# Performance work log

Measured on AMD Instinct MI355X. Metric: run time of the kernel, lower is better.

The kernel has to match this reference:

```python
import jax, jax.numpy as jnp
import numpy as np

L = 12; D = 768; H = 12; HD = D // H
P = 16; IMG = 224; NPATCH = (IMG // P) ** 2
NCLS = 1000; B = 32
GAMMA = 0.01; MIN_TOKENS = 16; EPS = 1e-6
SCALE = HD ** -0.5


def _ln(x, w, b, eps=1e-6):
    mu = x.mean(-1, keepdims=True)
    var = ((x - mu) ** 2).mean(-1, keepdims=True)
    return (x - mu) * jax.lax.rsqrt(var + eps) * w + b


def setup_inputs() -> dict:
    key = jax.random.key(0)
    ks = jax.random.split(key, 16)
    s = 0.02
    rn = lambda k, shape: jax.random.normal(k, shape, jnp.float32) * s
    return {
        'x': jax.random.normal(ks[0], (B, 3, IMG, IMG), jnp.float32),
        'patch_w': rn(ks[1], (D, 3, P, P)),
        'patch_b': jnp.zeros((D,), jnp.float32),
        'cls_token': rn(ks[2], (1, 1, D)),
        'pos_embed': rn(ks[3], (1, NPATCH + 1, D)),
        'ln1_w': jnp.ones((L, D), jnp.float32), 'ln1_b': jnp.zeros((L, D), jnp.float32),
        'qkv_w': rn(ks[4], (L, D, 3 * D)), 'qkv_b': jnp.zeros((L, 3 * D), jnp.float32),
        'proj_w': rn(ks[5], (L, D, D)), 'proj_b': jnp.zeros((L, D), jnp.float32),
        'ln2_w': jnp.ones((L, D), jnp.float32), 'ln2_b': jnp.zeros((L, D), jnp.float32),
        'fc1_w': rn(ks[6], (L, D, 4 * D)), 'fc1_b': jnp.zeros((L, 4 * D), jnp.float32),
        'fc2_w': rn(ks[7], (L, 4 * D, D)), 'fc2_b': jnp.zeros((L, D), jnp.float32),
        'norm_w': jnp.ones((D,), jnp.float32), 'norm_b': jnp.zeros((D,), jnp.float32),
        'head_w': rn(ks[8], (D, NCLS)), 'head_b': jnp.zeros((NCLS,), jnp.float32),
    }


def _block(x, i, ln1_w, ln1_b, qkv_w, qkv_b, proj_w, proj_b, ln2_w, ln2_b, fc1_w, fc1_b, fc2_w, fc2_b):
    Bb, Ntok, _ = x.shape
    xn = _ln(x, ln1_w[i], ln1_b[i])
    qkv = (xn @ qkv_w[i] + qkv_b[i]).reshape(Bb, Ntok, 3, H, HD)
    qkv = qkv.transpose(2, 0, 3, 1, 4)  # [3, B, H, N, hd]
    q, k, v = qkv[0], qkv[1], qkv[2]
    # full N x N attention matrix, materialized as in the original module
    attn = jax.nn.softmax(jnp.einsum('bhqd,bhkd->bhqk', q, k) * SCALE, axis=-1)
    out = jnp.einsum('bhqk,bhkd->bhqd', attn, v)
    out = out.transpose(0, 2, 1, 3).reshape(Bb, Ntok, D) @ proj_w[i] + proj_b[i]
    x = x + out
    h = _ln(x, ln2_w[i], ln2_b[i])
    h = jax.nn.gelu(h @ fc1_w[i] + fc1_b[i], approximate=False)
    x = x + (h @ fc2_w[i] + fc2_b[i])
    return x, attn, v


def _importance(attn, v, eps):
    # Jacobian proxy: d(CLS)/d(patch_j) ~ attn[CLS->j] * ||v_j||
    v_norm = jnp.linalg.norm(v, axis=-1)            # [B, H, N]
    jac = attn[:, :, 0, 1:] * v_norm[:, :, 1:]       # [B, H, Npatch]
    importance = jac.mean(axis=(0, 1))               # batch-shared [Npatch]
    mass = importance.sum()
    rho = importance.std() / (importance.mean() + eps)
    return importance, mass, rho


def _keep_ratio(rho, mass, prev_mass, gamma, eps):
    drift = jnp.abs(mass - prev_mass) / (prev_mass + eps)
    return jnp.clip(1.0 - gamma * rho * (1.0 + drift), 0.0, 1.0)


def _select(importance, n_keep):
    _, idx = jax.lax.top_k(importance, n_keep)
    idx = jnp.sort(idx) + 1  # shift past CLS
    return jnp.concatenate([jnp.zeros((1,), idx.dtype), idx])  # always keep CLS


def reference(x, patch_w, patch_b, cls_token, pos_embed, ln1_w, ln1_b, qkv_w, qkv_b,
              proj_w, proj_b, ln2_w, ln2_b, fc1_w, fc1_b, fc2_w, fc2_b,
              norm_w, norm_b, head_w, head_b):
    Bb = x.shape[0]
    feat = jax.lax.conv_general_dilated(x, patch_w, (P, P), 'VALID',
                                        dimension_numbers=('NCHW', 'OIHW', 'NCHW'))
    feat = feat.reshape(Bb, D, NPATCH).transpose(0, 2, 1) + patch_b  # [B, 196, D]
    xx = jnp.concatenate([jnp.broadcast_to(cls_token, (Bb, 1, D)), feat], axis=1) + pos_embed
    N = NPATCH
    prev_mass = None
    for i in range(L):
        xx, attn, v = _block(xx, i, ln1_w, ln1_b, qkv_w, qkv_b, proj_w, proj_b,
                             ln2_w, ln2_b, fc1_w, fc1_b, fc2_w, fc2_b)
        if N <= MIN_TOKENS:
            prev_mass = None
            continue
        imp, mass, rho = _importance(attn, v, EPS)
        if prev_mass is not None:
            kr = float(_keep_ratio(rho, mass, prev_mass, GAMMA, EPS))
            n_next = max(MIN_TOKENS, int(N * kr))
        else:
            n_next = N
        if n_next < N:
            keep_idx = _select(imp, n_next)
            xx = jnp.take(xx, keep_idx, axis=1)
            N = n_next
        prev_mass = mass
    xx = _ln(xx, norm_w, norm_b)
    return xx[:, 0] @ head_w + head_b
```

## Files before the change

### kernel.cpp

```cpp
#include <hip/hip_runtime.h>
#include <math.h>

#define DEV_INLINE __device__ __forceinline__

constexpr int BB     = 32;
constexpr int DMODEL = 768;
constexpr int NHEAD  = 12;
constexpr int NPATCH = 196;
constexpr int NTOK   = 197;
constexpr int NLAYER = 12;
constexpr int NCLASS = 1000;
constexpr int MTOT   = BB * NTOK;

typedef __attribute__((ext_vector_type(4))) float f32x4;
typedef __attribute__((ext_vector_type(8))) short bf16x8;

DEV_INLINE void split2(float x, unsigned short& hi, unsigned short& lo) {
    unsigned u = __builtin_bit_cast(unsigned, x);
    unsigned r = (u + 0x7FFFu + ((u >> 16) & 1u)) >> 16;
    hi = (unsigned short)r;
    float fh = __builtin_bit_cast(float, r << 16);
    float l = x - fh;
    unsigned ul = __builtin_bit_cast(unsigned, l);
    lo = (unsigned short)((ul + 0x7FFFu + ((ul >> 16) & 1u)) >> 16);
}

DEV_INLINE unsigned split_pack(float x) {
    unsigned short h, l; split2(x, h, l);
    return (unsigned)h | ((unsigned)l << 16);
}

DEV_INLINE void gload16(const unsigned short* g, unsigned short* l) {
    __builtin_amdgcn_global_load_lds(
        (const __attribute__((address_space(1))) unsigned int*)g,
        (__attribute__((address_space(3))) unsigned int*)l, 16, 0, 0);
}

DEV_INLINE float block_reduce_sum(float v, float* sbuf) {
    #pragma unroll
    for (int off = 32; off > 0; off >>= 1) v += __shfl_down(v, off, 64);
    int lane = threadIdx.x & 63, w = threadIdx.x >> 6;
    __syncthreads();
    if (lane == 0) sbuf[w] = v;
    __syncthreads();
    return sbuf[0] + sbuf[1] + sbuf[2] + sbuf[3];
}

__global__ void state_init(int* nTokPtr, int* prevValidPtr) {
    *nTokPtr = NTOK;
    *prevValidPtr = 0;
}

__global__ __launch_bounds__(256)
void cls_init(const float* __restrict__ cls, const float* __restrict__ pos,
              float* __restrict__ tok) {
    int b = blockIdx.x;
    for (int i = threadIdx.x; i < DMODEL; i += 256)
        tok[(size_t)b * NTOK * DMODEL + i] = cls[i] + pos[i];
}

__global__ __launch_bounds__(256)
void wconv_patch(const float* __restrict__ src, unsigned short* __restrict__ hi,
                 unsigned short* __restrict__ lo) {
    int id = blockIdx.x * 256 + threadIdx.x;
    if (id >= 768 * 96) return;
    int n = id / 96, ch = id % 96;
    int k = ch * 8;
    float4 a = *(const float4*)(src + (size_t)n * 768 + k);
    float4 b = *(const float4*)(src + (size_t)n * 768 + k + 4);
    unsigned short h[8], l[8];
    split2(a.x,h[0],l[0]); split2(a.y,h[1],l[1]); split2(a.z,h[2],l[2]); split2(a.w,h[3],l[3]);
    split2(b.x,h[4],l[4]); split2(b.y,h[5],l[5]); split2(b.z,h[6],l[6]); split2(b.w,h[7],l[7]);
    int npanel = n >> 7, c = n & 127;
    int kbi = k >> 5, chunk = (k >> 3) & 3;
    size_t base = ((size_t)npanel * 24 + kbi) * 4096
                + c * 32 + ((chunk ^ ((c >> 1) & 3)) << 3);
    bf16x8 hv, lv;
    #pragma unroll
    for (int j = 0; j < 8; ++j) { hv[j] = (short)h[j]; lv[j] = (short)l[j]; }
    *(bf16x8*)(hi + base) = hv;
    *(bf16x8*)(lo + base) = lv;
}

constexpr size_t WOFF_QKV  = 0;
constexpr size_t WOFF_PROJ = (size_t)768 * 2304;
constexpr size_t WOFF_FC1  = WOFF_PROJ + (size_t)768 * 768;
constexpr size_t WOFF_FC2  = WOFF_FC1 + (size_t)768 * 3072;
constexpr size_t WTOTAL    = WOFF_FC2 + (size_t)3072 * 768;

__global__ __launch_bounds__(256)
void wconv_layer(const float* __restrict__ qkvw, const float* __restrict__ projw,
                 const float* __restrict__ fc1w, const float* __restrict__ fc2w,
                 unsigned short* __restrict__ hi, unsigned short* __restrict__ lo) {
    __shared__ float tile[32][33];
    int bid = blockIdx.x;
    const float* src; int Kd, Nd; size_t dofs;
    if (bid < 1728)      { src = qkvw;  Kd = 768;  Nd = 2304; dofs = WOFF_QKV; }
    else if (bid < 2304) { bid -= 1728; src = projw; Kd = 768;  Nd = 768;  dofs = WOFF_PROJ; }
    else if (bid < 4608) { bid -= 2304; src = fc1w;  Kd = 768;  Nd = 3072; dofs = WOFF_FC1; }
    else                 { bid -= 4608; src = fc2w;  Kd = 3072; Nd = 768;  dofs = WOFF_FC2; }
    const int nkb = Kd >> 5;
    int ntx = Nd / 32;
    int n0 = (bid % ntx) * 32, k0 = (bid / ntx) * 32;
    int tx = threadIdx.x & 31, ty = threadIdx.x >> 5;
    #pragma unroll
    for (int i = 0; i < 32; i += 8)
        tile[ty + i][tx] = src[(size_t)(k0 + ty + i) * Nd + n0 + tx];
    __syncthreads();
    int t = threadIdx.x;
    if (t < 128) {
        int nl = t >> 2, chunk = t & 3;
        unsigned short h[8], l[8];
        #pragma unroll
        for (int j = 0; j < 8; ++j) split2(tile[chunk * 8 + j][nl], h[j], l[j]);
        int n = n0 + nl, k = k0 + chunk * 8;
        int npanel = n >> 7, c = n & 127;
        int kbi = k >> 5;
        size_t base = dofs + ((size_t)npanel * nkb + kbi) * 4096
                    + c * 32 + ((chunk ^ ((c >> 1) & 3)) << 3);
        bf16x8 hv, lv;
        #pragma unroll
        for (int j = 0; j < 8; ++j) { hv[j] = (short)h[j]; lv[j] = (short)l[j]; }
        *(bf16x8*)(hi + base) = hv;
        *(bf16x8*)(lo + base) = lv;
    }
}

template<int ASRC, int EPI>
__global__ __launch_bounds__(256)
void mfma_gemm(const void* __restrict__ A, int lda,
               const unsigned short* __restrict__ Wht,
               const unsigned short* __restrict__ Wlt,
               const float* __restrict__ bias,
               const float* __restrict__ resid,
               void* __restrict__ C, int ldc,
               int K, int Mtot, int gm, int gn,
               const int* __restrict__ nTokPtr) {
    const int nTok = (ASRC == 0) ? *nTokPtr : NTOK;
    int nb = gm * gn;
    int o = blockIdx.x;
    int q8 = nb >> 3, r8 = nb & 7;
    int xcd = o & 7, wi = o >> 3;
    int fin = (xcd < r8 ? xcd * (q8 + 1) : r8 * (q8 + 1) + (xcd - r8) * q8) + wi;
    int bm = fin / gn, bn = fin - bm * gn;
    const int m0 = bm * 128, n0 = bn * 128;
    if (m0 >= Mtot) return;
    if (ASRC == 0) {
        int ts = m0 % NTOK;
        if (!(ts < nTok || ts + 128 > NTOK)) return;
    }
    __shared__ unsigned short Ah[4096], Al[4096], Bh[4096], Bl[4096];
    const int tid = threadIdx.x;
    const int lane = tid & 63, wid = tid >> 6;
    const int wm = wid >> 1, wn = wid & 1;
    const int fr = lane & 15, fg = lane >> 4;

    f32x4 acc[4][4];
    #pragma unroll
    for (int i = 0; i < 4; ++i)
        #pragma unroll
        for (int j = 0; j < 4; ++j) acc[i][j] = (f32x4){0.f, 0.f, 0.f, 0.f};

    const int arow = tid >> 1;
    const int acp  = (tid & 1) * 2;
    const int am = m0 + arow;
    bool aval = am < Mtot;
    if (ASRC == 0) aval = aval && (am % NTOK) < nTok;
    size_t abase;
    if (ASRC == 0) abase = (size_t)am * lda;
    else {
        int b = am / NPATCH, pp = am - b * NPATCH;
        int py = pp / 14, px = pp - py * 14;
        abase = (size_t)b * (3 * 224 * 224) + (size_t)(py * 16) * 224 + px * 16;
    }
    const int axor = (arow >> 1) & 3;
    const int aoff0 = arow * 32 + ((acp ^ axor) << 3);
    const int aoff1 = arow * 32 + (((acp + 1) ^ axor) << 3);
    const int nkb = K >> 5;
    const int wbase = wid * 512;
    const int g8 = tid * 8;

    for (int kbi = 0; kbi < nkb; ++kbi) {
        const int kb = kbi << 5;
        {
            size_t tb = ((size_t)bn * nkb + kbi) * 4096;
            gload16(Wht + tb + g8,        &Bh[wbase]);
            gload16(Wht + tb + g8 + 2048, &Bh[wbase + 2048]);
            gload16(Wlt + tb + g8,        &Bl[wbase]);
            gload16(Wlt + tb + g8 + 2048, &Bl[wbase + 2048]);
        }
        unsigned ph[8], pl[8];
        if (ASRC == 0) {
            unsigned u[16] = {0,0,0,0,0,0,0,0,0,0,0,0,0,0,0,0};
            if (aval) {
                const unsigned* ap = (const unsigned*)A + abase + kb + acp * 8;
                *(uint4*)&u[0]  = *(const uint4*)ap;
                *(uint4*)&u[4]  = *(const uint4*)(ap + 4);
                *(uint4*)&u[8]  = *(const uint4*)(ap + 8);
                *(uint4*)&u[12] = *(const uint4*)(ap + 12);
            }
            #pragma unroll
            for (int j = 0; j < 8; ++j) {
                unsigned a = u[2 * j], b = u[2 * j + 1];
                ph[j] = (a & 0xffffu) | (b << 16);
                pl[j] = (a >> 16) | (b & 0xffff0000u);
            }
        } else {
            float f[16] = {0,0,0,0,0,0,0,0,0,0,0,0,0,0,0,0};
            if (aval) {
                int k = kb + acp * 8;
                size_t off = abase + (size_t)(k >> 8) * (224 * 224)
                           + (size_t)((k >> 4) & 15) * 224;
                *(float4*)&f[0]  = *(const float4*)((const float*)A + off);
                *(float4*)&f[4]  = *(const float4*)((const float*)A + off + 4);
                *(float4*)&f[8]  = *(const float4*)((const float*)A + off + 8);
                *(float4*)&f[12] = *(const float4*)((const float*)A + off + 12);
            }
            #pragma unroll
            for (int j = 0; j < 8; ++j) {
                unsigned short h0, l0, h1, l1;
                split2(f[2 * j], h0, l0); split2(f[2 * j + 1], h1, l1);
                ph[j] = (unsigned)h0 | ((unsigned)h1 << 16);
                pl[j] = (unsigned)l0 | ((unsigned)l1 << 16);
            }
        }
        *(uint4*)&Ah[aoff0] = *(uint4*)&ph[0];
        *(uint4*)&Ah[aoff1] = *(uint4*)&ph[4];
        *(uint4*)&Al[aoff0] = *(uint4*)&pl[0];
        *(uint4*)&Al[aoff1] = *(uint4*)&pl[4];
        __syncthreads();
        bf16x8 ah[4], al4[4], bh4[4], bl4[4];
        #pragma unroll
        for (int i = 0; i < 4; ++i) {
            int row = wm * 64 + i * 16 + fr;
            int aoff = row * 32 + ((fg ^ ((row >> 1) & 3)) << 3);
            ah[i]  = *(const bf16x8*)&Ah[aoff];
            al4[i] = *(const bf16x8*)&Al[aoff];
            int col = wn * 64 + i * 16 + fr;
            int boff = col * 32 + ((fg ^ ((col >> 1) & 3)) << 3);
            bh4[i] = *(const bf16x8*)&Bh[boff];
            bl4[i] = *(const bf16x8*)&Bl[boff];
        }
        #pragma unroll
        for (int i = 0; i < 4; ++i)
            #pragma unroll
            for (int j = 0; j < 4; ++j) {
                acc[i][j] = __builtin_amdgcn_mfma_f32_16x16x32_bf16(ah[i],  bh4[j], acc[i][j], 0, 0, 0);
                acc[i][j] = __builtin_amdgcn_mfma_f32_16x16x32_bf16(ah[i],  bl4[j], acc[i][j], 0, 0, 0);
                acc[i][j] = __builtin_amdgcn_mfma_f32_16x16x32_bf16(al4[i], bh4[j], acc[i][j], 0, 0, 0);
            }
        __syncthreads();
    }
    #pragma unroll
    for (int i = 0; i < 4; ++i) {
        #pragma unroll
        for (int j = 0; j < 4; ++j) {
            #pragma unroll
            for (int e = 0; e < 4; ++e) {
                int m = m0 + wm * 64 + i * 16 + fg * 4 + e;
                int n = n0 + wn * 64 + j * 16 + fr;
                if (m >= Mtot) continue;
                if (ASRC == 0 && (m % NTOK) >= nTok) continue;
                float v = acc[i][j][e] + bias[n];
                if constexpr (EPI == 0) {
                    ((unsigned*)C)[(size_t)m * ldc + n] = split_pack(v);
                } else if constexpr (EPI == 1) {
                    ((float*)C)[(size_t)m * ldc + n] = v + resid[(size_t)m * ldc + n];
                } else if constexpr (EPI == 2) {
                    v = 0.5f * v * (1.0f + erff(v * 0.70710678118654752f));
                    ((unsigned*)C)[(size_t)m * ldc + n] = split_pack(v);
                } else {
                    int b = m / NPATCH, pp = m - b * NPATCH;
                    v += resid[(size_t)(1 + pp) * DMODEL + n];
                    ((float*)C)[((size_t)b * NTOK + 1 + pp) * DMODEL + n] = v;
                }
            }
        }
    }
}

__global__ __launch_bounds__(256)
void ln_tok(const float* __restrict__ X, unsigned* __restrict__ Y,
            const float* __restrict__ w, const float* __restrict__ b,
            const int* __restrict__ nTokPtr) {
    int m = blockIdx.x;
    if ((m % NTOK) >= *nTokPtr) return;
    __shared__ float sbuf[4];
    const float* x = X + (size_t)m * DMODEL;
    int tid = threadIdx.x;
    float v[3];
    #pragma unroll
    for (int i = 0; i < 3; i++) v[i] = x[tid + i * 256];
    float mu = block_reduce_sum(v[0] + v[1] + v[2], sbuf) * (1.0f / 768.0f);
    float d2 = 0.f;
    #pragma unroll
    for (int i = 0; i < 3; i++) { float d = v[i] - mu; d2 = fmaf(d, d, d2); }
    float var = block_reduce_sum(d2, sbuf) * (1.0f / 768.0f);
    float rstd = rsqrtf(var + 1e-6f);
    #pragma unroll
    for (int i = 0; i < 3; i++) {
        int idx = tid + i * 256;
        float y = (v[i] - mu) * rstd * w[idx] + b[idx];
        Y[(size_t)m * DMODEL + idx] = split_pack(y);
    }
}

__global__ __launch_bounds__(256)
void ln_cls(const float* __restrict__ X, float* __restrict__ Y,
            const float* __restrict__ w, const float* __restrict__ b) {
    int bb = blockIdx.x;
    __shared__ float sbuf[4];
    const float* x = X + (size_t)bb * NTOK * DMODEL;
    int tid = threadIdx.x;
    float v[3];
    #pragma unroll
    for (int i = 0; i < 3; i++) v[i] = x[tid + i * 256];
    float mu = block_reduce_sum(v[0] + v[1] + v[2], sbuf) * (1.0f / 768.0f);
    float d2 = 0.f;
    #pragma unroll
    for (int i = 0; i < 3; i++) { float d = v[i] - mu; d2 = fmaf(d, d, d2); }
    float var = block_reduce_sum(d2, sbuf) * (1.0f / 768.0f);
    float rstd = rsqrtf(var + 1e-6f);
    #pragma unroll
    for (int i = 0; i < 3; i++) {
        int idx = tid + i * 256;
        Y[(size_t)bb * DMODEL + idx] = (v[i] - mu) * rstd * w[idx] + b[idx];
    }
}

__global__ __launch_bounds__(256)
void attn_v3(const unsigned* __restrict__ qkv, unsigned* __restrict__ outu,
             float* __restrict__ jacg, const int* __restrict__ nTokPtr) {
    const int nTok = *nTokPtr;
    const int bh = blockIdx.x;
    const int b = bh / NHEAD, h = bh % NHEAD;
    const int q0 = blockIdx.y * 32;
    if (q0 >= nTok) return;
    __shared__ unsigned short Kh[64 * 64], Kl[64 * 64];
    __shared__ unsigned short Vth[64 * 64], Vtl[64 * 64];
    __shared__ unsigned short Ph[32 * 64], Pl[32 * 64];
    __shared__ float Ss[32][68];
    __shared__ float mrow[32], lrow[32], frow[32];
    __shared__ float s0row[256], vnrow[256];
    __shared__ float vnpart[64][4];
    const int tid = threadIdx.x;
    const int lane = tid & 63, wv = tid >> 6;
    const int fr = lane & 15, fg = lane >> 4;
    const int qh = wv >> 1, xh = wv & 1;
    const unsigned* base = qkv + (size_t)b * NTOK * 2304 + (size_t)h * 64;

    {
        unsigned* Qu = (unsigned*)&Ss[0][0];
        int r = tid >> 3, fc = tid & 7;
        int q = q0 + r;
        uint4 v = make_uint4(0,0,0,0), w = make_uint4(0,0,0,0);
        if (q < nTok) {
            v = *(const uint4*)(base + (size_t)q * 2304 + fc * 8);
            w = *(const uint4*)(base + (size_t)q * 2304 + fc * 8 + 4);
        }
        *(uint4*)&Qu[r * 68 + fc * 8] = v;
        *(uint4*)&Qu[r * 68 + fc * 8 + 4] = w;
    }
    if (tid < 32) { mrow[tid] = -INFINITY; lrow[tid] = 0.f; frow[tid] = 1.f; }
    __syncthreads();
    bf16x8 qah[2], qal[2];
    {
        const unsigned* Qu = (const unsigned*)&Ss[0][0];
        int r = qh * 16 + fr;
        #pragma unroll
        for (int s = 0; s < 2; ++s)
            #pragma unroll
            for (int i = 0; i < 8; ++i) {
                unsigned u = Qu[r * 68 + s * 32 + fg * 8 + i];
                qah[s][i] = (short)(u & 0xffffu);
                qal[s][i] = (short)(u >> 16);
            }
    }
    f32x4 oacc[2] = {{0,0,0,0},{0,0,0,0}};
    const int njt = (nTok + 63) >> 6;
    const int sj = tid & 63, sdh = tid >> 6;

    for (int jt = 0; jt < njt; ++jt) {
        const int jb = jt * 64;
        __syncthreads();
        {
            int j = jb + sj;
            uint4 ku[4], vu[4];
            if (j < nTok) {
                const unsigned* kr = base + (size_t)j * 2304 + 768 + sdh * 16;
                const unsigned* vr = base + (size_t)j * 2304 + 1536 + sdh * 16;
                ku[0] = *(const uint4*)kr;       ku[1] = *(const uint4*)(kr + 4);
                ku[2] = *(const uint4*)(kr + 8); ku[3] = *(const uint4*)(kr + 12);
                vu[0] = *(const uint4*)vr;       vu[1] = *(const uint4*)(vr + 4);
                vu[2] = *(const uint4*)(vr + 8); vu[3] = *(const uint4*)(vr + 12);
            } else {
                ku[0]=ku[1]=ku[2]=ku[3] = make_uint4(0,0,0,0);
                vu[0]=vu[1]=vu[2]=vu[3] = make_uint4(0,0,0,0);
            }
            const unsigned* kw = (const unsigned*)ku;
            bf16x8 kh0, kh1, kl0, kl1;
            #pragma unroll
            for (int i = 0; i < 8; ++i) {
                kh0[i] = (short)(kw[i] & 0xffffu);     kl0[i] = (short)(kw[i] >> 16);
                kh1[i] = (short)(kw[8 + i] & 0xffffu); kl1[i] = (short)(kw[8 + i] >> 16);
            }
            int c0 = sdh * 2;
            int ko0 = sj * 64 + ((c0 ^ (sj & 7)) << 3);
            int ko1 = sj * 64 + (((c0 + 1) ^ (sj & 7)) << 3);
            *(bf16x8*)&Kh[ko0] = kh0; *(bf16x8*)&Kh[ko1] = kh1;
            *(bf16x8*)&Kl[ko0] = kl0; *(bf16x8*)&Kl[ko1] = kl1;
            const unsigned* vw = (const unsigned*)vu;
            float pn = 0.f;
            #pragma unroll
            for (int i = 0; i < 16; ++i) {
                unsigned u = vw[i];
                int d = sdh * 16 + i;
                int si = d * 64 + (((sj >> 3) ^ (d & 7)) << 3) + (sj & 7);
                Vth[si] = (unsigned short)(u & 0xffffu);
                Vtl[si] = (unsigned short)(u >> 16);
                if (q0 == 0) {
                    float vf = __builtin_bit_cast(float, u << 16)
                             + __builtin_bit_cast(float, u & 0xffff0000u);
                    pn = fmaf(vf, vf, pn);
                }
            }
            if (q0 == 0) vnpart[sj][sdh] = pn;
        }
        __syncthreads();
        {
            f32x4 sacc[2] = {{0,0,0,0},{0,0,0,0}};
            #pragma unroll
            for (int s = 0; s < 2; ++s)
                #pragma unroll
                for (int t = 0; t < 2; ++t) {
                    int j = xh * 32 + t * 16 + fr;
                    int off = j * 64 + (((s * 4 + fg) ^ (j & 7)) << 3);
                    bf16x8 kbh = *(const bf16x8*)&Kh[off];
                    bf16x8 kbl = *(const bf16x8*)&Kl[off];
                    sacc[t] = __builtin_amdgcn_mfma_f32_16x16x32_bf16(qah[s], kbh, sacc[t], 0, 0, 0);
                    sacc[t] = __builtin_amdgcn_mfma_f32_16x16x32_bf16(qah[s], kbl, sacc[t], 0, 0, 0);
                    sacc[t] = __builtin_amdgcn_mfma_f32_16x16x32_bf16(qal[s], kbh, sacc[t], 0, 0, 0);
                }
            #pragma unroll
            for (int t = 0; t < 2; ++t)
                #pragma unroll
                for (int e = 0; e < 4; ++e) {
                    int q = q0 + qh * 16 + fg * 4 + e;
                    int j = jb + xh * 32 + t * 16 + fr;
                    Ss[qh * 16 + fg * 4 + e][xh * 32 + t * 16 + fr] =
                        (q < nTok && j < nTok) ? sacc[t][e] * 0.125f : -INFINITY;
                }
        }
        __syncthreads();
        {
            int q = tid >> 3, s = tid & 7;
            bool rowok = (q0 + q) < nTok;
            float4 va = *(const float4*)&Ss[q][s * 8];
            float4 vb = *(const float4*)&Ss[q][s * 8 + 4];
            if (q0 == 0 && q == 0) {
                *(float4*)&s0row[jb + s * 8] = va;
                *(float4*)&s0row[jb + s * 8 + 4] = vb;
            }
            float mx = fmaxf(fmaxf(fmaxf(va.x, va.y), fmaxf(va.z, va.w)),
                             fmaxf(fmaxf(vb.x, vb.y), fmaxf(vb.z, vb.w)));
            #pragma unroll
            for (int o = 1; o < 8; o <<= 1) mx = fmaxf(mx, __shfl_xor(mx, o));
            float mold = mrow[q];
            float mnew = fmaxf(mold, mx);
            float e[8];
            float sum = 0.f;
            if (rowok) {
                e[0] = expf(va.x - mnew); e[1] = expf(va.y - mnew);
                e[2] = expf(va.z - mnew); e[3] = expf(va.w - mnew);
                e[4] = expf(vb.x - mnew); e[5] = expf(vb.y - mnew);
                e[6] = expf(vb.z - mnew); e[7] = expf(vb.w - mnew);
                sum = ((e[0] + e[1]) + (e[2] + e[3])) + ((e[4] + e[5]) + (e[6] + e[7]));
            } else {
                #pragma unroll
                for (int i = 0; i < 8; ++i) e[i] = 0.f;
            }
            #pragma unroll
            for (int o = 1; o < 8; o <<= 1) sum += __shfl_xor(sum, o);
            bf16x8 ph, pl;
            #pragma unroll
            for (int i = 0; i < 8; ++i) {
                unsigned u = __builtin_bit_cast(unsigned, e[i]);
                ph[i] = (short)(u >> 16);
                float r = e[i] - __builtin_bit_cast(float, u & 0xffff0000u);
                pl[i] = (short)(__builtin_bit_cast(unsigned, r) >> 16);
            }
            int poff = q * 64 + ((s ^ (q & 7)) << 3);
            *(bf16x8*)&Ph[poff] = ph;
            *(bf16x8*)&Pl[poff] = pl;
            if (s == 0 && rowok) {
                float f = expf(mold - mnew);
                lrow[q] = lrow[q] * f + sum;
                mrow[q] = mnew;
                frow[q] = f;
            }
            if (q0 == 0 && tid < 64) {
                int jj = jb + tid;
                if (jj < nTok)
                    vnrow[jj] = sqrtf(vnpart[tid][0] + vnpart[tid][1]
                                    + vnpart[tid][2] + vnpart[tid][3]);
            }
        }
        __syncthreads();
        {
            float fe[4];
            #pragma unroll
            for (int e = 0; e < 4; ++e) fe[e] = frow[qh * 16 + fg * 4 + e];
            #pragma unroll
            for (int t = 0; t < 2; ++t)
                #pragma unroll
                for (int e = 0; e < 4; ++e) oacc[t][e] *= fe[e];
            #pragma unroll
            for (int s = 0; s < 2; ++s) {
                int pr = qh * 16 + fr;
                int poff = pr * 64 + (((s * 4 + fg) ^ (pr & 7)) << 3);
                bf16x8 pah = *(const bf16x8*)&Ph[poff];
                bf16x8 pal = *(const bf16x8*)&Pl[poff];
                #pragma unroll
                for (int t = 0; t < 2; ++t) {
                    int d = xh * 32 + t * 16 + fr;
                    int voff = d * 64 + (((s * 4 + fg) ^ (d & 7)) << 3);
                    bf16x8 vbh = *(const bf16x8*)&Vth[voff];
                    bf16x8 vbl = *(const bf16x8*)&Vtl[voff];
                    oacc[t] = __builtin_amdgcn_mfma_f32_16x16x32_bf16(pah, vbh, oacc[t], 0, 0, 0);
                    oacc[t] = __builtin_amdgcn_mfma_f32_16x16x32_bf16(pah, vbl, oacc[t], 0, 0, 0);
                    oacc[t] = __builtin_amdgcn_mfma_f32_16x16x32_bf16(pal, vbh, oacc[t], 0, 0, 0);
                }
            }
        }
    }
    #pragma unroll
    for (int e = 0; e < 4; ++e) {
        int qr = qh * 16 + fg * 4 + e;
        int q = q0 + qr;
        if (q < nTok) {
            float inv = 1.0f / lrow[qr];
            #pragma unroll
            for (int t = 0; t < 2; ++t) {
                int n = h * 64 + xh * 32 + t * 16 + fr;
                outu[((size_t)b * NTOK + q) * DMODEL + n] = split_pack(oacc[t][e] * inv);
            }
        }
    }
    if (q0 == 0) {
        float m0f = mrow[0], l0 = lrow[0];
        for (int j = 1 + tid; j < nTok; j += 256)
            jacg[(size_t)bh * NPATCH + (j - 1)] = (expf(s0row[j] - m0f) / l0) * vnrow[j];
    }
}

__global__ __launch_bounds__(256)
void decide_kernel(const float* __restrict__ jac,
                   int* __restrict__ nTokPtr, int* __restrict__ nTokNextPtr,
                   int* __restrict__ keepIdx, float* __restrict__ prevMassPtr,
                   int* __restrict__ prevValidPtr) {
    const int nTok = *nTokPtr;
    const int N = nTok - 1;
    const int tid = threadIdx.x;
    if (N <= 16) {
        if (tid == 0) { *prevValidPtr = 0; *nTokNextPtr = nTok; }
        for (int t = tid; t < nTok; t += 256) keepIdx[t] = t;
        return;
    }
    __shared__ float impF[NPATCH];
    __shared__ int   sel[NPATCH];
    __shared__ int   s_next;
    for (int j = tid; j < N; j += 256) {
        double s = 0.0;
        for (int r = 0; r < BB * NHEAD; r++) s += (double)jac[(size_t)r * NPATCH + j];
        impF[j] = (float)(s * (1.0 / 384.0));
    }
    __syncthreads();
    if (tid == 0) {
        double ms = 0.0;
        for (int j = 0; j < N; j++) ms += (double)impF[j];
        float massF = (float)ms;
        float meanF = (float)(ms / (double)N);
        double vs = 0.0;
        for (int j = 0; j < N; j++) { double d = (double)impF[j] - (double)meanF; vs += d * d; }
        float stdF = (float)sqrt(vs / (double)N);
        float rho = stdF / (meanF + 1e-6f);
        int nnext;
        if (*prevValidPtr != 0) {
            float pm = *prevMassPtr;
            float drift = fabsf(massF - pm) / (pm + 1e-6f);
            float kr = 1.0f - 0.01f * rho * (1.0f + drift);
            kr = fminf(fmaxf(kr, 0.0f), 1.0f);
            int t = (int)((double)N * (double)kr);
            nnext = t < 16 ? 16 : t;
        } else {
            nnext = N;
        }
        *prevMassPtr = massF;
        *prevValidPtr = 1;
        s_next = nnext;
        *nTokNextPtr = nnext + 1;
    }
    __syncthreads();
    int nnext = s_next;
    if (nnext < N) {
        for (int j = tid; j < N; j += 256) {
            float vj = impF[j];
            int rank = 0;
            for (int i = 0; i < N; i++) {
                float vi = impF[i];
                rank += (vi > vj || (vi == vj && i < j)) ? 1 : 0;
            }
            sel[j] = (rank < nnext) ? 1 : 0;
        }
        __syncthreads();
        if (tid == 0) {
            int c = 1;
            keepIdx[0] = 0;
            for (int j = 0; j < N; j++) if (sel[j]) keepIdx[c++] = j + 1;
        }
    } else {
        for (int t = tid; t < nTok; t += 256) keepIdx[t] = t;
    }
}

__global__ __launch_bounds__(192)
void gather_kernel(const float* __restrict__ src, float* __restrict__ dst,
                   const int* __restrict__ keepIdx,
                   const int* __restrict__ nTokNextPtr, int* __restrict__ nTokPtr) {
    int nn = *nTokNextPtr;
    int m = blockIdx.x;
    int b = m / NTOK, t = m - b * NTOK;
    if (t < nn) {
        int s = keepIdx[t];
        const float4* sp = (const float4*)(src + ((size_t)b * NTOK + s) * DMODEL);
        float4* dp = (float4*)(dst + ((size_t)b * NTOK + t) * DMODEL);
        dp[threadIdx.x] = sp[threadIdx.x];
    }
    if (m == 0 && threadIdx.x == 0) *nTokPtr = nn;
}

__global__ __launch_bounds__(256)
void head_kernel(const float* __restrict__ lnC, const float* __restrict__ W,
                 const float* __restrict__ hb, float* __restrict__ out) {
    int b = blockIdx.x;
    int n = blockIdx.y * 256 + threadIdx.x;
    __shared__ float xs[DMODEL];
    for (int i = threadIdx.x; i < DMODEL; i += 256) xs[i] = lnC[(size_t)b * DMODEL + i];
    __syncthreads();
    if (n < NCLASS) {
        float acc = hb[n];
        for (int d = 0; d < DMODEL; d++) acc = fmaf(xs[d], W[(size_t)d * NCLASS + n], acc);
        out[(size_t)b * NCLASS + n] = acc;
    }
}

extern "C" void kernel_launch(void* const* d_in, const int* in_sizes, int n_in,
                              void* d_out, int out_size, void* d_ws, size_t ws_size,
                              hipStream_t stream) {
    const float* x       = (const float*)d_in[0];
    const float* patch_w = (const float*)d_in[1];
    const float* patch_b = (const float*)d_in[2];
    const float* cls_tok = (const float*)d_in[3];
    const float* pos     = (const float*)d_in[4];
    const float* ln1_w   = (const float*)d_in[5];
    const float* ln1_b   = (const float*)d_in[6];
    const float* qkv_w   = (const float*)d_in[7];
    const float* qkv_b   = (const float*)d_in[8];
    const float* proj_w  = (const float*)d_in[9];
    const float* proj_b  = (const float*)d_in[10];
    const float* ln2_w   = (const float*)d_in[11];
    const float* ln2_b   = (const float*)d_in[12];
    const float* fc1_w   = (const float*)d_in[13];
    const float* fc1_b   = (const float*)d_in[14];
    const float* fc2_w   = (const float*)d_in[15];
    const float* fc2_b   = (const float*)d_in[16];
    const float* norm_w  = (const float*)d_in[17];
    const float* norm_b  = (const float*)d_in[18];
    const float* head_w  = (const float*)d_in[19];
    const float* head_b  = (const float*)d_in[20];
    float* out = (float*)d_out;

    char* ws = (char*)d_ws;
    size_t off = 0;
    auto alloc = [&](size_t nbytes) {
        char* p = ws + off;
        off += ((nbytes + 255) / 256) * 256;
        return p;
    };
    float* tokA = (float*)alloc((size_t)MTOT * DMODEL * 4);
    float* tokB = (float*)alloc((size_t)MTOT * DMODEL * 4);
    char* uni = alloc((size_t)MTOT * 3072 * 4);
    unsigned* qkvb = (unsigned*)uni;
    unsigned* hbu = (unsigned*)uni;
    unsigned* xnu  = (unsigned*)alloc((size_t)MTOT * DMODEL * 4);
    unsigned* outu = (unsigned*)alloc((size_t)MTOT * DMODEL * 4);
    unsigned short* whi = (unsigned short*)alloc(WTOTAL * 2);
    unsigned short* wlo = (unsigned short*)alloc(WTOTAL * 2);
    unsigned short* wphi = (unsigned short*)alloc((size_t)768 * 768 * 2);
    unsigned short* wplo = (unsigned short*)alloc((size_t)768 * 768 * 2);
    float* jac  = (float*)alloc((size_t)BB * NHEAD * NPATCH * 4);
    float* lnC  = (float*)alloc((size_t)BB * DMODEL * 4);
    float* prevMass = (float*)alloc(32);
    int* ints = (int*)alloc(1024);
    int* nTokP = ints; int* nTokNextP = ints + 1; int* prevValidP = ints + 2;
    int* keepIdx = ints + 4;

    dim3 blk(256);
    state_init<<<dim3(1), dim3(1), 0, stream>>>(nTokP, prevValidP);
    wconv_patch<<<dim3(288), blk, 0, stream>>>(patch_w, wphi, wplo);
    cls_init<<<dim3(BB), blk, 0, stream>>>(cls_tok, pos, tokA);
    mfma_gemm<1, 3><<<dim3(49 * 6), blk, 0, stream>>>(
        x, 0, wphi, wplo, patch_b, pos, tokA, DMODEL, 768, BB * NPATCH, 49, 6, nTokP);

    float* bufs[2] = {tokA, tokB};
    const int gm = (MTOT + 127) / 128;
    for (int l = 0; l < NLAYER; l++) {
        float* cur = bufs[l & 1];
        float* nxt = bufs[(l + 1) & 1];
        wconv_layer<<<dim3(6912), blk, 0, stream>>>(
            qkv_w + (size_t)l * 768 * 2304, proj_w + (size_t)l * 768 * 768,
            fc1_w + (size_t)l * 768 * 3072, fc2_w + (size_t)l * 3072 * 768, whi, wlo);
        ln_tok<<<dim3(MTOT), blk, 0, stream>>>(cur, xnu, ln1_w + l * 768, ln1_b + l * 768, nTokP);
        mfma_gemm<0, 0><<<dim3(gm * 18), blk, 0, stream>>>(
            xnu, 768, whi + WOFF_QKV, wlo + WOFF_QKV, qkv_b + (size_t)l * 2304,
            nullptr, qkvb, 2304, 768, MTOT, gm, 18, nTokP);
        attn_v3<<<dim3(BB * NHEAD, 7), blk, 0, stream>>>(qkvb, outu, jac, nTokP);
        mfma_gemm<0, 1><<<dim3(gm * 6), blk, 0, stream>>>(
            outu, 768, whi + WOFF_PROJ, wlo + WOFF_PROJ, proj_b + (size_t)l * 768,
            cur, cur, 768, 768, MTOT, gm, 6, nTokP);
        ln_tok<<<dim3(MTOT), blk, 0, stream>>>(cur, xnu, ln2_w + l * 768, ln2_b + l * 768, nTokP);
        mfma_gemm<0, 2><<<dim3(gm * 24), blk, 0, stream>>>(
            xnu, 768, whi + WOFF_FC1, wlo + WOFF_FC1, fc1_b + (size_t)l * 3072,
            nullptr, hbu, 3072, 768, MTOT, gm, 24, nTokP);
        mfma_gemm<0, 1><<<dim3(gm * 6), blk, 0, stream>>>(
            hbu, 3072, whi + WOFF_FC2, wlo + WOFF_FC2, fc2_b + (size_t)l * 768,
            cur, cur, 768, 3072, MTOT, gm, 6, nTokP);
        decide_kernel<<<dim3(1), blk, 0, stream>>>(jac, nTokP, nTokNextP, keepIdx,
                                                   prevMass, prevValidP);
        gather_kernel<<<dim3(MTOT), dim3(192), 0, stream>>>(cur, nxt, keepIdx, nTokNextP, nTokP);
    }
    ln_cls<<<dim3(BB), blk, 0, stream>>>(bufs[0], lnC, norm_w, norm_b);
    head_kernel<<<dim3(BB, 4), blk, 0, stream>>>(lnC, head_w, head_b, out);
}
```

Before: 6.455 ms.

## Store activations as pre-swizzled split bf16 planes and DMA A tiles into LDS

Activations (LN outputs, attention outputs, FC1 outputs, QKV) are now stored as separate hi/lo bf16 planes instead of interleaved packed words. LN, attention and FC1 outputs are written in the GEMM's LDS swizzle order, so the A operand can be loaded with global_load_lds DMA instead of register loads plus unpacking. GEMM epilogues for the bf16 outputs go through LDS so stores are coalesced 16-byte writes. Buffers are padded to a multiple of 128 rows so A tiles can be loaded without bounds checks. The aim is to cut global-load instruction overhead and the unpack work in the GEMM A path. The cost is extra LDS round trips and barriers in the epilogue, and the padded rows are read without masking.

```diff
diff --git a/kernel.cpp b/kernel.cpp
--- a/kernel.cpp
+++ b/kernel.cpp
@@ -11,6 +11,7 @@
 constexpr int NLAYER = 12;
 constexpr int NCLASS = 1000;
 constexpr int MTOT   = BB * NTOK;
+constexpr int MPAD   = 6400;
 
 typedef __attribute__((ext_vector_type(4))) float f32x4;
 typedef __attribute__((ext_vector_type(8))) short bf16x8;
@@ -30,10 +31,18 @@
     return (unsigned)h | ((unsigned)l << 16);
 }
 
+DEV_INLINE float bf2f(unsigned short s) {
+    return __builtin_bit_cast(float, ((unsigned)s) << 16);
+}
+
 DEV_INLINE void gload16(const unsigned short* g, unsigned short* l) {
     __builtin_amdgcn_global_load_lds(
         (const __attribute__((address_space(1))) unsigned int*)g,
         (__attribute__((address_space(3))) unsigned int*)l, 16, 0, 0);
+}
+
+DEV_INLINE int aswz(int m, int k) {
+    return (k & ~31) + ((((k >> 3) & 3) ^ ((m >> 1) & 3)) << 3) + (k & 7);
 }
 
 DEV_INLINE float block_reduce_sum(float v, float* sbuf) {
@@ -128,20 +137,22 @@
 
 template<int ASRC, int EPI>
 __global__ __launch_bounds__(256)
-void mfma_gemm(const void* __restrict__ A, int lda,
+void mfma_gemm(const unsigned short* __restrict__ Ahp,
+               const unsigned short* __restrict__ Alp,
+               const float* __restrict__ Af,
                const unsigned short* __restrict__ Wht,
                const unsigned short* __restrict__ Wlt,
                const float* __restrict__ bias,
                const float* __restrict__ resid,
-               void* __restrict__ C, int ldc,
-               int K, int Mtot, int gm, int gn,
+               void* __restrict__ C, void* __restrict__ C2,
+               int ldc, int K, int Mtot, int gm, int gn,
                const int* __restrict__ nTokPtr) {
     const int nTok = (ASRC == 0) ? *nTokPtr : NTOK;
     int nb = gm * gn;
     int o = blockIdx.x;
-    int q8 = nb >> 3, r8 = nb & 7;
+    int qd = nb >> 3, r8 = nb & 7;
     int xcd = o & 7, wi = o >> 3;
-    int fin = (xcd < r8 ? xcd * (q8 + 1) : r8 * (q8 + 1) + (xcd - r8) * q8) + wi;
+    int fin = (xcd < r8 ? xcd * (qd + 1) : r8 * (qd + 1) + (xcd - r8) * qd) + wi;
     int bm = fin / gn, bn = fin - bm * gn;
     const int m0 = bm * 128, n0 = bn * 128;
     if (m0 >= Mtot) return;
@@ -149,7 +160,11 @@
         int ts = m0 % NTOK;
         if (!(ts < nTok || ts + 128 > NTOK)) return;
     }
-    __shared__ unsigned short Ah[4096], Al[4096], Bh[4096], Bl[4096];
+    __shared__ unsigned short LDSu[16384];
+    unsigned short* AhL = LDSu;
+    unsigned short* AlL = LDSu + 4096;
+    unsigned short* BhL = LDSu + 8192;
+    unsigned short* BlL = LDSu + 12288;
     const int tid = threadIdx.x;
     const int lane = tid & 63, wid = tid >> 6;
     const int wm = wid >> 1, wn = wid & 1;
@@ -161,61 +176,55 @@
         #pragma unroll
         for (int j = 0; j < 4; ++j) acc[i][j] = (f32x4){0.f, 0.f, 0.f, 0.f};
 
-    const int arow = tid >> 1;
-    const int acp  = (tid & 1) * 2;
-    const int am = m0 + arow;
-    bool aval = am < Mtot;
-    if (ASRC == 0) aval = aval && (am % NTOK) < nTok;
-    size_t abase;
-    if (ASRC == 0) abase = (size_t)am * lda;
-    else {
+    const int nkb = K >> 5;
+    const int wbase = wid * 512;
+    const int g8 = tid * 8;
+
+    int arow = 0, acp = 0, axor = 0, aoff0 = 0, aoff1 = 0;
+    bool aval = false; size_t abase = 0;
+    if constexpr (ASRC == 1) {
+        arow = tid >> 1;
+        acp  = (tid & 1) * 2;
+        int am = m0 + arow;
+        aval = am < Mtot;
         int b = am / NPATCH, pp = am - b * NPATCH;
         int py = pp / 14, px = pp - py * 14;
         abase = (size_t)b * (3 * 224 * 224) + (size_t)(py * 16) * 224 + px * 16;
-    }
-    const int axor = (arow >> 1) & 3;
-    const int aoff0 = arow * 32 + ((acp ^ axor) << 3);
-    const int aoff1 = arow * 32 + (((acp + 1) ^ axor) << 3);
-    const int nkb = K >> 5;
-    const int wbase = wid * 512;
-    const int g8 = tid * 8;
+        axor = (arow >> 1) & 3;
+        aoff0 = arow * 32 + ((acp ^ axor) << 3);
+        aoff1 = arow * 32 + (((acp + 1) ^ axor) << 3);
+    }
+    size_t arow_g = 0;
+    if constexpr (ASRC == 0)
+        arow_g = (size_t)(m0 + (tid >> 2)) * K + (tid & 3) * 8;
 
     for (int kbi = 0; kbi < nkb; ++kbi) {
-        const int kb = kbi << 5;
         {
-            size_t tb = ((size_t)bn * nkb + kbi) * 4096;
-            gload16(Wht + tb + g8,        &Bh[wbase]);
-            gload16(Wht + tb + g8 + 2048, &Bh[wbase + 2048]);
-            gload16(Wlt + tb + g8,        &Bl[wbase]);
-            gload16(Wlt + tb + g8 + 2048, &Bl[wbase + 2048]);
-        }
-        unsigned ph[8], pl[8];
-        if (ASRC == 0) {
-            unsigned u[16] = {0,0,0,0,0,0,0,0,0,0,0,0,0,0,0,0};
-            if (aval) {
-                const unsigned* ap = (const unsigned*)A + abase + kb + acp * 8;
-                *(uint4*)&u[0]  = *(const uint4*)ap;
-                *(uint4*)&u[4]  = *(const uint4*)(ap + 4);
-                *(uint4*)&u[8]  = *(const uint4*)(ap + 8);
-                *(uint4*)&u[12] = *(const uint4*)(ap + 12);
-            }
-            #pragma unroll
-            for (int j = 0; j < 8; ++j) {
-                unsigned a = u[2 * j], b = u[2 * j + 1];
-                ph[j] = (a & 0xffffu) | (b << 16);
-                pl[j] = (a >> 16) | (b & 0xffff0000u);
-            }
+            size_t tb = ((size_t)bn * nkb + kbi) * 4096 + g8;
+            gload16(Wht + tb,        &BhL[wbase]);
+            gload16(Wht + tb + 2048, &BhL[wbase + 2048]);
+            gload16(Wlt + tb,        &BlL[wbase]);
+            gload16(Wlt + tb + 2048, &BlL[wbase + 2048]);
+        }
+        if constexpr (ASRC == 0) {
+            size_t ab = arow_g + (size_t)kbi * 32;
+            gload16(Ahp + ab,                  &AhL[wbase]);
+            gload16(Ahp + ab + (size_t)64 * K, &AhL[wbase + 2048]);
+            gload16(Alp + ab,                  &AlL[wbase]);
+            gload16(Alp + ab + (size_t)64 * K, &AlL[wbase + 2048]);
         } else {
+            const int kb = kbi << 5;
             float f[16] = {0,0,0,0,0,0,0,0,0,0,0,0,0,0,0,0};
             if (aval) {
                 int k = kb + acp * 8;
                 size_t off = abase + (size_t)(k >> 8) * (224 * 224)
                            + (size_t)((k >> 4) & 15) * 224;
-                *(float4*)&f[0]  = *(const float4*)((const float*)A + off);
-                *(float4*)&f[4]  = *(const float4*)((const float*)A + off + 4);
-                *(float4*)&f[8]  = *(const float4*)((const float*)A + off + 8);
-                *(float4*)&f[12] = *(const float4*)((const float*)A + off + 12);
-            }
+                *(float4*)&f[0]  = *(const float4*)(Af + off);
+                *(float4*)&f[4]  = *(const float4*)(Af + off + 4);
+                *(float4*)&f[8]  = *(const float4*)(Af + off + 8);
+                *(float4*)&f[12] = *(const float4*)(Af + off + 12);
+            }
+            unsigned ph[8], pl[8];
             #pragma unroll
             for (int j = 0; j < 8; ++j) {
                 unsigned short h0, l0, h1, l1;
@@ -223,23 +232,23 @@
                 ph[j] = (unsigned)h0 | ((unsigned)h1 << 16);
                 pl[j] = (unsigned)l0 | ((unsigned)l1 << 16);
             }
-        }
-        *(uint4*)&Ah[aoff0] = *(uint4*)&ph[0];
-        *(uint4*)&Ah[aoff1] = *(uint4*)&ph[4];
-        *(uint4*)&Al[aoff0] = *(uint4*)&pl[0];
-        *(uint4*)&Al[aoff1] = *(uint4*)&pl[4];
+            *(uint4*)&AhL[aoff0] = *(uint4*)&ph[0];
+            *(uint4*)&AhL[aoff1] = *(uint4*)&ph[4];
+            *(uint4*)&AlL[aoff0] = *(uint4*)&pl[0];
+            *(uint4*)&AlL[aoff1] = *(uint4*)&pl[4];
+        }
         __syncthreads();
         bf16x8 ah[4], al4[4], bh4[4], bl4[4];
         #pragma unroll
         for (int i = 0; i < 4; ++i) {
             int row = wm * 64 + i * 16 + fr;
             int aoff = row * 32 + ((fg ^ ((row >> 1) & 3)) << 3);
-            ah[i]  = *(const bf16x8*)&Ah[aoff];
-            al4[i] = *(const bf16x8*)&Al[aoff];
+            ah[i]  = *(const bf16x8*)&AhL[aoff];
+            al4[i] = *(const bf16x8*)&AlL[aoff];
             int col = wn * 64 + i * 16 + fr;
             int boff = col * 32 + ((fg ^ ((col >> 1) & 3)) << 3);
-            bh4[i] = *(const bf16x8*)&Bh[boff];
-            bl4[i] = *(const bf16x8*)&Bl[boff];
+            bh4[i] = *(const bf16x8*)&BhL[boff];
+            bl4[i] = *(const bf16x8*)&BlL[boff];
         }
         #pragma unroll
         for (int i = 0; i < 4; ++i)
@@ -251,41 +260,84 @@
             }
         __syncthreads();
     }
-    #pragma unroll
-    for (int i = 0; i < 4; ++i) {
-        #pragma unroll
-        for (int j = 0; j < 4; ++j) {
-            #pragma unroll
-            for (int e = 0; e < 4; ++e) {
-                int m = m0 + wm * 64 + i * 16 + fg * 4 + e;
-                int n = n0 + wn * 64 + j * 16 + fr;
-                if (m >= Mtot) continue;
-                if (ASRC == 0 && (m % NTOK) >= nTok) continue;
-                float v = acc[i][j][e] + bias[n];
-                if constexpr (EPI == 0) {
-                    ((unsigned*)C)[(size_t)m * ldc + n] = split_pack(v);
-                } else if constexpr (EPI == 1) {
-                    ((float*)C)[(size_t)m * ldc + n] = v + resid[(size_t)m * ldc + n];
-                } else if constexpr (EPI == 2) {
-                    v = 0.5f * v * (1.0f + erff(v * 0.70710678118654752f));
-                    ((unsigned*)C)[(size_t)m * ldc + n] = split_pack(v);
-                } else {
-                    int b = m / NPATCH, pp = m - b * NPATCH;
-                    v += resid[(size_t)(1 + pp) * DMODEL + n];
-                    ((float*)C)[((size_t)b * NTOK + 1 + pp) * DMODEL + n] = v;
+    if constexpr (EPI == 0 || EPI == 2) {
+        unsigned pk[4][4][4];
+        #pragma unroll
+        for (int i = 0; i < 4; ++i)
+            #pragma unroll
+            for (int j = 0; j < 4; ++j)
+                #pragma unroll
+                for (int e = 0; e < 4; ++e) {
+                    int n = n0 + wn * 64 + j * 16 + fr;
+                    float v = acc[i][j][e] + bias[n];
+                    if constexpr (EPI == 2)
+                        v = 0.5f * v * (1.0f + erff(v * 0.70710678118654752f));
+                    pk[i][j][e] = split_pack(v);
                 }
-            }
-        }
+        const int rr = tid >> 4, cc = tid & 15;
+        #pragma unroll
+        for (int plane = 0; plane < 2; ++plane) {
+            __syncthreads();
+            #pragma unroll
+            for (int i = 0; i < 4; ++i)
+                #pragma unroll
+                for (int j = 0; j < 4; ++j)
+                    #pragma unroll
+                    for (int e = 0; e < 4; ++e) {
+                        int r = wm * 64 + i * 16 + fg * 4 + e;
+                        int c = wn * 64 + j * 16 + fr;
+                        LDSu[r * 128 + c] = (unsigned short)
+                            (plane ? (pk[i][j][e] >> 16) : (pk[i][j][e] & 0xffffu));
+                    }
+            __syncthreads();
+            unsigned short* Cp = (unsigned short*)(plane ? C2 : C);
+            #pragma unroll
+            for (int p = 0; p < 8; ++p) {
+                int r = p * 16 + rr;
+                int m = m0 + r;
+                if (m < Mtot && (m % NTOK) < nTok) {
+                    size_t dst;
+                    if constexpr (EPI == 0)
+                        dst = (size_t)m * ldc + n0 + cc * 8;
+                    else
+                        dst = (size_t)m * ldc + n0 + (cc >> 2) * 32
+                            + (((cc & 3) ^ ((m >> 1) & 3)) << 3);
+                    *(bf16x8*)(Cp + dst) = *(const bf16x8*)&LDSu[r * 128 + cc * 8];
+                }
+            }
+        }
+    } else {
+        #pragma unroll
+        for (int i = 0; i < 4; ++i)
+            #pragma unroll
+            for (int j = 0; j < 4; ++j)
+                #pragma unroll
+                for (int e = 0; e < 4; ++e) {
+                    int m = m0 + wm * 64 + i * 16 + fg * 4 + e;
+                    int n = n0 + wn * 64 + j * 16 + fr;
+                    if (m >= Mtot) continue;
+                    if (ASRC == 0 && (m % NTOK) >= nTok) continue;
+                    float v = acc[i][j][e] + bias[n];
+                    if constexpr (EPI == 1) {
+                        ((float*)C)[(size_t)m * ldc + n] = v + resid[(size_t)m * ldc + n];
+                    } else {
+                        int b = m / NPATCH, pp = m - b * NPATCH;
+                        v += resid[(size_t)(1 + pp) * DMODEL + n];
+                        ((float*)C)[((size_t)b * NTOK + 1 + pp) * DMODEL + n] = v;
+                    }
+                }
     }
 }
 
 __global__ __launch_bounds__(256)
-void ln_tok(const float* __restrict__ X, unsigned* __restrict__ Y,
+void ln_tok(const float* __restrict__ X, unsigned short* __restrict__ Yh,
+            unsigned short* __restrict__ Yl,
             const float* __restrict__ w, const float* __restrict__ b,
             const int* __restrict__ nTokPtr) {
     int m = blockIdx.x;
     if ((m % NTOK) >= *nTokPtr) return;
     __shared__ float sbuf[4];
+    __shared__ float yb[768];
     const float* x = X + (size_t)m * DMODEL;
     int tid = threadIdx.x;
     float v[3];
@@ -300,8 +352,20 @@
     #pragma unroll
     for (int i = 0; i < 3; i++) {
         int idx = tid + i * 256;
-        float y = (v[i] - mu) * rstd * w[idx] + b[idx];
-        Y[(size_t)m * DMODEL + idx] = split_pack(y);
+        yb[idx] = (v[i] - mu) * rstd * w[idx] + b[idx];
+    }
+    __syncthreads();
+    if (tid < 96) {
+        bf16x8 hv, lv;
+        #pragma unroll
+        for (int j = 0; j < 8; ++j) {
+            unsigned short h, l; split2(yb[tid * 8 + j], h, l);
+            hv[j] = (short)h; lv[j] = (short)l;
+        }
+        size_t dst = (size_t)m * 768 + (tid >> 2) * 32
+                   + (((tid & 3) ^ ((m >> 1) & 3)) << 3);
+        *(bf16x8*)(Yh + dst) = hv;
+        *(bf16x8*)(Yl + dst) = lv;
     }
 }
 
@@ -329,7 +393,10 @@
 }
 
 __global__ __launch_bounds__(256)
-void attn_v3(const unsigned* __restrict__ qkv, unsigned* __restrict__ outu,
+void attn_v4(const unsigned short* __restrict__ qh_g,
+             const unsigned short* __restrict__ ql_g,
+             unsigned short* __restrict__ oh_g,
+             unsigned short* __restrict__ ol_g,
              float* __restrict__ jacg, const int* __restrict__ nTokPtr) {
     const int nTok = *nTokPtr;
     const int bh = blockIdx.x;
@@ -347,35 +414,20 @@
     const int lane = tid & 63, wv = tid >> 6;
     const int fr = lane & 15, fg = lane >> 4;
     const int qh = wv >> 1, xh = wv & 1;
-    const unsigned* base = qkv + (size_t)b * NTOK * 2304 + (size_t)h * 64;
-
-    {
-        unsigned* Qu = (unsigned*)&Ss[0][0];
-        int r = tid >> 3, fc = tid & 7;
-        int q = q0 + r;
-        uint4 v = make_uint4(0,0,0,0), w = make_uint4(0,0,0,0);
-        if (q < nTok) {
-            v = *(const uint4*)(base + (size_t)q * 2304 + fc * 8);
-            w = *(const uint4*)(base + (size_t)q * 2304 + fc * 8 + 4);
-        }
-        *(uint4*)&Qu[r * 68 + fc * 8] = v;
-        *(uint4*)&Qu[r * 68 + fc * 8 + 4] = w;
-    }
-    if (tid < 32) { mrow[tid] = -INFINITY; lrow[tid] = 0.f; frow[tid] = 1.f; }
-    __syncthreads();
+
     bf16x8 qah[2], qal[2];
     {
-        const unsigned* Qu = (const unsigned*)&Ss[0][0];
-        int r = qh * 16 + fr;
-        #pragma unroll
-        for (int s = 0; s < 2; ++s)
-            #pragma unroll
-            for (int i = 0; i < 8; ++i) {
-                unsigned u = Qu[r * 68 + s * 32 + fg * 8 + i];
-                qah[s][i] = (short)(u & 0xffffu);
-                qal[s][i] = (short)(u >> 16);
-            }
-    }
+        int q = q0 + qh * 16 + fr;
+        int qe = q < nTok ? q : nTok - 1;
+        const unsigned short* qrh = qh_g + (size_t)(b * NTOK + qe) * 2304 + h * 64;
+        const unsigned short* qrl = ql_g + (size_t)(b * NTOK + qe) * 2304 + h * 64;
+        #pragma unroll
+        for (int s = 0; s < 2; ++s) {
+            qah[s] = *(const bf16x8*)(qrh + s * 32 + fg * 8);
+            qal[s] = *(const bf16x8*)(qrl + s * 32 + fg * 8);
+        }
+    }
+    if (tid < 32) { mrow[tid] = -INFINITY; lrow[tid] = 0.f; frow[tid] = 1.f; }
     f32x4 oacc[2] = {{0,0,0,0},{0,0,0,0}};
     const int njt = (nTok + 63) >> 6;
     const int sj = tid & 63, sdh = tid >> 6;
@@ -385,42 +437,36 @@
         __syncthreads();
         {
             int j = jb + sj;
-            uint4 ku[4], vu[4];
+            bf16x8 kh0, kh1, kl0, kl1, vh0, vh1, vl0, vl1;
             if (j < nTok) {
-                const unsigned* kr = base + (size_t)j * 2304 + 768 + sdh * 16;
-                const unsigned* vr = base + (size_t)j * 2304 + 1536 + sdh * 16;
-                ku[0] = *(const uint4*)kr;       ku[1] = *(const uint4*)(kr + 4);
-                ku[2] = *(const uint4*)(kr + 8); ku[3] = *(const uint4*)(kr + 12);
-                vu[0] = *(const uint4*)vr;       vu[1] = *(const uint4*)(vr + 4);
-                vu[2] = *(const uint4*)(vr + 8); vu[3] = *(const uint4*)(vr + 12);
+                size_t rp = (size_t)(b * NTOK + j) * 2304 + h * 64;
+                kh0 = *(const bf16x8*)(qh_g + rp + 768 + sdh * 16);
+                kh1 = *(const bf16x8*)(qh_g + rp + 768 + sdh * 16 + 8);
+                kl0 = *(const bf16x8*)(ql_g + rp + 768 + sdh * 16);
+                kl1 = *(const bf16x8*)(ql_g + rp + 768 + sdh * 16 + 8);
+                vh0 = *(const bf16x8*)(qh_g + rp + 1536 + sdh * 16);
+                vh1 = *(const bf16x8*)(qh_g + rp + 1536 + sdh * 16 + 8);
+                vl0 = *(const bf16x8*)(ql_g + rp + 1536 + sdh * 16);
+                vl1 = *(const bf16x8*)(ql_g + rp + 1536 + sdh * 16 + 8);
             } else {
-                ku[0]=ku[1]=ku[2]=ku[3] = make_uint4(0,0,0,0);
-                vu[0]=vu[1]=vu[2]=vu[3] = make_uint4(0,0,0,0);
-            }
-            const unsigned* kw = (const unsigned*)ku;
-            bf16x8 kh0, kh1, kl0, kl1;
-            #pragma unroll
-            for (int i = 0; i < 8; ++i) {
-                kh0[i] = (short)(kw[i] & 0xffffu);     kl0[i] = (short)(kw[i] >> 16);
-                kh1[i] = (short)(kw[8 + i] & 0xffffu); kl1[i] = (short)(kw[8 + i] >> 16);
+                bf16x8 z = {0,0,0,0,0,0,0,0};
+                kh0=kh1=kl0=kl1=vh0=vh1=vl0=vl1 = z;
             }
             int c0 = sdh * 2;
             int ko0 = sj * 64 + ((c0 ^ (sj & 7)) << 3);
             int ko1 = sj * 64 + (((c0 + 1) ^ (sj & 7)) << 3);
             *(bf16x8*)&Kh[ko0] = kh0; *(bf16x8*)&Kh[ko1] = kh1;
             *(bf16x8*)&Kl[ko0] = kl0; *(bf16x8*)&Kl[ko1] = kl1;
-            const unsigned* vw = (const unsigned*)vu;
             float pn = 0.f;
             #pragma unroll
             for (int i = 0; i < 16; ++i) {
-                unsigned u = vw[i];
+                unsigned short vh = (unsigned short)(i < 8 ? vh0[i] : vh1[i - 8]);
+                unsigned short vl = (unsigned short)(i < 8 ? vl0[i] : vl1[i - 8]);
                 int d = sdh * 16 + i;
                 int si = d * 64 + (((sj >> 3) ^ (d & 7)) << 3) + (sj & 7);
-                Vth[si] = (unsigned short)(u & 0xffffu);
-                Vtl[si] = (unsigned short)(u >> 16);
+                Vth[si] = vh; Vtl[si] = vl;
                 if (q0 == 0) {
-                    float vf = __builtin_bit_cast(float, u << 16)
-                             + __builtin_bit_cast(float, u & 0xffff0000u);
+                    float vf = bf2f(vh) + bf2f(vl);
                     pn = fmaf(vf, vf, pn);
                 }
             }
@@ -539,10 +585,16 @@
         int q = q0 + qr;
         if (q < nTok) {
             float inv = 1.0f / lrow[qr];
+            int m = b * NTOK + q;
+            int xr = (m >> 1) & 3;
             #pragma unroll
             for (int t = 0; t < 2; ++t) {
                 int n = h * 64 + xh * 32 + t * 16 + fr;
-                outu[((size_t)b * NTOK + q) * DMODEL + n] = split_pack(oacc[t][e] * inv);
+                unsigned short hh, ll;
+                split2(oacc[t][e] * inv, hh, ll);
+                size_t dst = (size_t)m * 768 + (n & ~31)
+                           + ((((n >> 3) & 3) ^ xr) << 3) + (n & 7);
+                oh_g[dst] = hh; ol_g[dst] = ll;
             }
         }
     }
@@ -689,13 +741,17 @@
     };
     float* tokA = (float*)alloc((size_t)MTOT * DMODEL * 4);
     float* tokB = (float*)alloc((size_t)MTOT * DMODEL * 4);
-    char* uni = alloc((size_t)MTOT * 3072 * 4);
-    unsigned* qkvb = (unsigned*)uni;
-    unsigned* hbu = (unsigned*)uni;
-    unsigned* xnu  = (unsigned*)alloc((size_t)MTOT * DMODEL * 4);
-    unsigned* outu = (unsigned*)alloc((size_t)MTOT * DMODEL * 4);
-    unsigned short* whi = (unsigned short*)alloc(WTOTAL * 2);
-    unsigned short* wlo = (unsigned short*)alloc(WTOTAL * 2);
+    char* uni = alloc((size_t)2 * MPAD * 3072 * 2);
+    unsigned short* qkvh = (unsigned short*)uni;
+    unsigned short* qkvl = qkvh + (size_t)MTOT * 2304;
+    unsigned short* hbh  = (unsigned short*)uni;
+    unsigned short* hbl  = hbh + (size_t)MPAD * 3072;
+    unsigned short* xnh  = (unsigned short*)alloc((size_t)MPAD * DMODEL * 2);
+    unsigned short* xnl  = (unsigned short*)alloc((size_t)MPAD * DMODEL * 2);
+    unsigned short* outh = (unsigned short*)alloc((size_t)MPAD * DMODEL * 2);
+    unsigned short* outl = (unsigned short*)alloc((size_t)MPAD * DMODEL * 2);
+    unsigned short* whi  = (unsigned short*)alloc(WTOTAL * 2);
+    unsigned short* wlo  = (unsigned short*)alloc(WTOTAL * 2);
     unsigned short* wphi = (unsigned short*)alloc((size_t)768 * 768 * 2);
     unsigned short* wplo = (unsigned short*)alloc((size_t)768 * 768 * 2);
     float* jac  = (float*)alloc((size_t)BB * NHEAD * NPATCH * 4);
@@ -710,31 +766,34 @@
     wconv_patch<<<dim3(288), blk, 0, stream>>>(patch_w, wphi, wplo);
     cls_init<<<dim3(BB), blk, 0, stream>>>(cls_tok, pos, tokA);
     mfma_gemm<1, 3><<<dim3(49 * 6), blk, 0, stream>>>(
-        x, 0, wphi, wplo, patch_b, pos, tokA, DMODEL, 768, BB * NPATCH, 49, 6, nTokP);
+        nullptr, nullptr, x, wphi, wplo, patch_b, pos, tokA, nullptr,
+        DMODEL, 768, BB * NPATCH, 49, 6, nTokP);
 
     float* bufs[2] = {tokA, tokB};
-    const int gm = (MTOT + 127) / 128;
+    const int gm = MPAD / 128;
     for (int l = 0; l < NLAYER; l++) {
         float* cur = bufs[l & 1];
         float* nxt = bufs[(l + 1) & 1];
         wconv_layer<<<dim3(6912), blk, 0, stream>>>(
             qkv_w + (size_t)l * 768 * 2304, proj_w + (size_t)l * 768 * 768,
             fc1_w + (size_t)l * 768 * 3072, fc2_w + (size_t)l * 3072 * 768, whi, wlo);
-        ln_tok<<<dim3(MTOT), blk, 0, stream>>>(cur, xnu, ln1_w + l * 768, ln1_b + l * 768, nTokP);
+        ln_tok<<<dim3(MTOT), blk, 0, stream>>>(cur, xnh, xnl,
+            ln1_w + l * 768, ln1_b + l * 768, nTokP);
         mfma_gemm<0, 0><<<dim3(gm * 18), blk, 0, stream>>>(
-            xnu, 768, whi + WOFF_QKV, wlo + WOFF_QKV, qkv_b + (size_t)l * 2304,
-            nullptr, qkvb, 2304, 768, MTOT, gm, 18, nTokP);
-        attn_v3<<<dim3(BB * NHEAD, 7), blk, 0, stream>>>(qkvb, outu, jac, nTokP);
+            xnh, xnl, nullptr, whi + WOFF_QKV, wlo + WOFF_QKV, qkv_b + (size_t)l * 2304,
+            nullptr, qkvh, qkvl, 2304, 768, MTOT, gm, 18, nTokP);
+        attn_v4<<<dim3(BB * NHEAD, 7), blk, 0, stream>>>(qkvh, qkvl, outh, outl, jac, nTokP);
         mfma_gemm<0, 1><<<dim3(gm * 6), blk, 0, stream>>>(
-            outu, 768, whi + WOFF_PROJ, wlo + WOFF_PROJ, proj_b + (size_t)l * 768,
-            cur, cur, 768, 768, MTOT, gm, 6, nTokP);
-        ln_tok<<<dim3(MTOT), blk, 0, stream>>>(cur, xnu, ln2_w + l * 768, ln2_b + l * 768, nTokP);
+            outh, outl, nullptr, whi + WOFF_PROJ, wlo + WOFF_PROJ, proj_b + (size_t)l * 768,
+            cur, cur, nullptr, 768, 768, MTOT, gm, 6, nTokP);
+        ln_tok<<<dim3(MTOT), blk, 0, stream>>>(cur, xnh, xnl,
+            ln2_w + l * 768, ln2_b + l * 768, nTokP);
         mfma_gemm<0, 2><<<dim3(gm * 24), blk, 0, stream>>>(
-            xnu, 768, whi + WOFF_FC1, wlo + WOFF_FC1, fc1_b + (size_t)l * 3072,
-            nullptr, hbu, 3072, 768, MTOT, gm, 24, nTokP);
+            xnh, xnl, nullptr, whi + WOFF_FC1, wlo + WOFF_FC1, fc1_b + (size_t)l * 3072,
+            nullptr, hbh, hbl, 3072, 768, MTOT, gm, 24, nTokP);
         mfma_gemm<0, 1><<<dim3(gm * 6), blk, 0, stream>>>(
-            hbu, 3072, whi + WOFF_FC2, wlo + WOFF_FC2, fc2_b + (size_t)l * 768,
-            cur, cur, 768, 3072, MTOT, gm, 6, nTokP);
+            hbh, hbl, nullptr, whi + WOFF_FC2, wlo + WOFF_FC2, fc2_b + (size_t)l * 768,
+            cur, cur, nullptr, 768, 3072, MTOT, gm, 6, nTokP);
         decide_kernel<<<dim3(1), blk, 0, stream>>>(jac, nTokP, nTokNextP, keepIdx,
                                                    prevMass, prevValidP);
         gather_kernel<<<dim3(MTOT), dim3(192), 0, stream>>>(cur, nxt, keepIdx, nTokNextP, nTokP);
```

New measurement: 7.198 ms. 11.5% more time.
